# Kernel optimization log

Measured on AMD Instinct MI355X. Metric: run time of the kernel, lower is better.

The kernel has to match this reference:

```python
import jax, jax.numpy as jnp
import numpy as np

D_MODEL = 1024
NUM_HEADS = 16
HEAD_DIM = D_MODEL // NUM_HEADS


def setup_inputs() -> dict:
    key = jax.random.key(0)
    ks = jax.random.split(key, 11)
    B, S, D = 2, 2048, D_MODEL
    scale = 1.0 / np.sqrt(D)
    inp = {
        "query": jax.random.normal(ks[0], (B, S, D), jnp.float32),
        "key": jax.random.normal(ks[1], (B, S, D), jnp.float32),
        "value": jax.random.normal(ks[2], (B, S, D), jnp.float32),
        "Wq": jax.random.normal(ks[3], (D, D), jnp.float32) * scale,
        "bq": jnp.zeros((D,), jnp.float32),
        "Wk": jax.random.normal(ks[4], (D, D), jnp.float32) * scale,
        "bk": jnp.zeros((D,), jnp.float32),
        "Wv": jax.random.normal(ks[5], (D, D), jnp.float32) * scale,
        "bv": jnp.zeros((D,), jnp.float32),
        "Wo": jax.random.normal(ks[6], (D, D), jnp.float32) * scale,
        "bo": jnp.zeros((D,), jnp.float32),
    }
    return inp


def reference(query, key, value, Wq, bq, Wk, bk, Wv, bv, Wo, bo):
    B, S, D = query.shape
    H, hd = NUM_HEADS, HEAD_DIM
    # linear projections (x @ W^T + b, torch nn.Linear convention)
    Q = query @ Wq.T + bq
    K = key @ Wk.T + bk
    V = value @ Wv.T + bv
    # split heads: [B, S, H, hd] -> [B, H, S, hd]
    Q = Q.reshape(B, S, H, hd).transpose(0, 2, 1, 3)
    K = K.reshape(B, S, H, hd).transpose(0, 2, 1, 3)
    V = V.reshape(B, S, H, hd).transpose(0, 2, 1, 3)
    # scaled dot-product attention (explicit, non-flash)
    scores = jnp.einsum("bhqd,bhkd->bhqk", Q, K) / jnp.sqrt(jnp.float32(hd)).astype(Q.dtype)
    attn = jax.nn.softmax(scores, axis=-1)
    out = jnp.einsum("bhqk,bhkd->bhqd", attn, V)
    # merge heads: [B, H, S, hd] -> [B, S, D]
    out = out.transpose(0, 2, 1, 3).reshape(B, S, D)
    return out @ Wo.T + bo
```

## Files before the change

### kernel.cpp

```cpp
#include <hip/hip_runtime.h>
#include <hip/hip_bf16.h>


constexpr int D_MODEL = 1024;
constexpr int S_LEN   = 2048;
constexpr int BATCH   = 2;
constexpr int NH      = 16;
constexpr int HD      = 64;
constexpr int ROWS    = BATCH * S_LEN;

typedef __attribute__((ext_vector_type(8))) short short8;
typedef __attribute__((ext_vector_type(4))) float float4a;

static __device__ __forceinline__ unsigned short f2bf(float f) {
  union { float f; unsigned u; } v{f};
  unsigned r = v.u + 0x7FFFu + ((v.u >> 16) & 1u);
  return (unsigned short)(r >> 16);
}

static __device__ __forceinline__ unsigned pack_bf16(float a, float b) {
#if __has_builtin(__builtin_amdgcn_cvt_pk_bf16_f32)
  typedef __attribute__((ext_vector_type(2))) __bf16 bf16x2;
  union { bf16x2 v; unsigned u; } c;
  c.v = __builtin_amdgcn_cvt_pk_bf16_f32(a, b);
  return c.u;
#else
  return (unsigned)f2bf(a) | ((unsigned)f2bf(b) << 16);
#endif
}

static __device__ __forceinline__ float bf2f(unsigned short u) {
  union { unsigned u; float f; } v;
  v.u = (unsigned)u << 16;
  return v.f;
}

static __device__ __forceinline__ void async16(const void* g, void* l) {
  __builtin_amdgcn_global_load_lds(
      (const __attribute__((address_space(1))) unsigned int*)g,
      (__attribute__((address_space(3))) unsigned int*)l, 16, 0, 0);
}

struct ConvArgs { const float* s[7]; unsigned short* d[7]; int n[7]; };

__global__ __launch_bounds__(256) void convert_bf16(ConvArgs a) {
  const int which = blockIdx.y;
  const int i = (blockIdx.x * 256 + threadIdx.x) * 8;
  if (i >= a.n[which]) return;
  const float4* s = (const float4*)(a.s[which] + i);
  float4 x = s[0], y = s[1];
  unsigned t[4] = {pack_bf16(x.x, x.y), pack_bf16(x.z, x.w),
                   pack_bf16(y.x, y.y), pack_bf16(y.z, y.w)};
  *(short8*)(a.d[which] + i) = *(short8*)t;
}

template <int MODE>
static __device__ __forceinline__ void gemm_body(
    const unsigned short* __restrict__ A, const unsigned short* __restrict__ W,
    const float* __restrict__ bias, void* __restrict__ Yv, float scale,
    unsigned short* As, unsigned short* Bs, unsigned short* Tb) {
  const int tid = threadIdx.x;
  const int w = tid >> 6, lane = tid & 63;
  const int l15 = lane & 15, quad = lane >> 4;
  const int row0 = blockIdx.x * 128, col0 = blockIdx.y * 128;
  const int wm = (w & 1) * 64, wn = (w >> 1) * 64;

  float4a acc[4][4];
#pragma unroll
  for (int i = 0; i < 4; i++)
#pragma unroll
    for (int j = 0; j < 4; j++) acc[i][j] = (float4a){0.f, 0.f, 0.f, 0.f};

  const int swA = (quad + (wm >> 1) + (l15 >> 1)) & 3;
  const int swB = (quad + (wn >> 1) + (l15 >> 1)) & 3;

  for (int kt = 0; kt < D_MODEL; kt += 32) {
    __syncthreads();
#pragma unroll
    for (int j = 0; j < 2; j++) {
      const int i = w * 2 + j;
      const int r = i * 16 + (lane >> 2);
      const int c = ((lane & 3) - (r >> 1)) & 3;
      async16(W + (size_t)(col0 + r) * D_MODEL + kt + c * 8, (char*)Bs + i * 1024);
      async16(A + (size_t)(row0 + r) * D_MODEL + kt + c * 8, (char*)As + i * 1024);
    }
    __syncthreads();

    short8 af[4], bf[4];
#pragma unroll
    for (int mt = 0; mt < 4; mt++) {
      const int r = wm + mt * 16 + l15;
      af[mt] = *(const short8*)&As[(r * 4 + swA) * 8];
    }
#pragma unroll
    for (int nt = 0; nt < 4; nt++) {
      const int r = wn + nt * 16 + l15;
      bf[nt] = *(const short8*)&Bs[(r * 4 + swB) * 8];
    }
#pragma unroll
    for (int mt = 0; mt < 4; mt++)
#pragma unroll
      for (int nt = 0; nt < 4; nt++)
        acc[mt][nt] = __builtin_amdgcn_mfma_f32_16x16x32_bf16(af[mt], bf[nt], acc[mt][nt], 0, 0, 0);
  }

  int cols[4];
  float bvs[4];
#pragma unroll
  for (int nt = 0; nt < 4; nt++) {
    cols[nt] = col0 + wn + nt * 16 + l15;
    bvs[nt]  = bias[cols[nt]] * ((MODE == 0) ? scale : 1.0f);
  }

  if constexpr (MODE == 0) {
    unsigned short* Y = (unsigned short*)Yv;
#pragma unroll
    for (int mt = 0; mt < 4; mt++)
#pragma unroll
      for (int r = 0; r < 4; r++) {
        const int m = row0 + wm + mt * 16 + quad * 4 + r;
        const int bb = m >> 11, s = m & 2047;
#pragma unroll
        for (int nt = 0; nt < 4; nt++) {
          const int h = cols[nt] >> 6, d = cols[nt] & 63;
          Y[(((size_t)(bb * NH + h)) * S_LEN + s) * HD + d] =
              f2bf(acc[mt][nt][r] * scale + bvs[nt]);
        }
      }
  } else {
    __syncthreads();
    unsigned short* T = Tb + w * (64 * 32);
    unsigned short* Y = (unsigned short*)Yv;
#pragma unroll
    for (int p = 0; p < 2; p++) {
      if (p) { asm volatile("s_waitcnt lgkmcnt(0)" ::: "memory"); }
#pragma unroll
      for (int mi = 0; mi < 2; mi++) {
        const int mt = 2 * p + mi;
#pragma unroll
        for (int r = 0; r < 4; r++) {
          const int sl = mi * 16 + quad * 4 + r;
          const int cch = sl >> 3;
#pragma unroll
          for (int nt = 0; nt < 4; nt++) {
            const int dl = nt * 16 + l15;
            const int slot = cch ^ (dl & 3);
            T[dl * 32 + slot * 8 + (sl & 7)] = f2bf(acc[mt][nt][r] + bvs[nt]);
          }
        }
      }
      asm volatile("s_waitcnt lgkmcnt(0)" ::: "memory");
#pragma unroll
      for (int j = 0; j < 4; j++) {
        const int cid = j * 64 + lane;
        const int dl = cid >> 2;
        const int c  = cid & 3;
        const int slot = c ^ (dl & 3);
        short8 v = *(const short8*)&T[dl * 32 + slot * 8];
        const int col = col0 + wn + dl;
        const int h = col >> 6, d = col & 63;
        const int m = row0 + wm + p * 32 + c * 8;
        const int bb = m >> 11, s = m & 2047;
        *(short8*)&Y[(((size_t)(bb * NH + h)) * HD + d) * S_LEN + s] = v;
      }
    }
  }
}

__global__ __launch_bounds__(256) void gemm_qkv(
    const unsigned short* xq, const unsigned short* xk, const unsigned short* xv,
    const unsigned short* wq, const unsigned short* wk, const unsigned short* wv,
    const float* bq, const float* bk, const float* bv,
    unsigned short* Q, unsigned short* K, unsigned short* Vt) {
  __shared__ unsigned short smem[2 * 128 * 32];
  unsigned short* As = smem;
  unsigned short* Bs = smem + 128 * 32;
  unsigned short* Tb = smem;
  const int z = blockIdx.z;
  if (z == 0)      gemm_body<0>(xq, wq, bq, Q,  0.125f * 1.44269504f, As, Bs, Tb);
  else if (z == 1) gemm_body<0>(xk, wk, bk, K,  1.0f, As, Bs, Tb);
  else             gemm_body<2>(xv, wv, bv, Vt, 1.0f, As, Bs, Tb);
}

__global__ __launch_bounds__(256) void gemm_o(
    const unsigned short* __restrict__ Op, const float* __restrict__ Lp,
    const unsigned short* __restrict__ wo, const float* __restrict__ bo,
    float* __restrict__ out) {
  __shared__ unsigned short As[64 * 32];
  __shared__ unsigned short Bs[128 * 32];
  const int tid = threadIdx.x;
  const int w = tid >> 6, lane = tid & 63;
  const int l15 = lane & 15, quad = lane >> 4;
  const int row0 = blockIdx.x * 64, col0 = blockIdx.y * 128;
  const int wn = w * 32;

  const int ar = w * 16 + (lane >> 2);
  const int cg = lane & 3;
  const int asl = (cg + (ar >> 1)) & 3;
  const int grow = row0 + ar;
  const unsigned short* P0 = Op + (size_t)grow * D_MODEL + cg * 8;
  const unsigned short* P1 = P0 + (size_t)ROWS * D_MODEL;
  const float* L0 = Lp + (size_t)grow * NH;
  const float* L1 = L0 + (size_t)ROWS * NH;

  float4a acc[4][2];
#pragma unroll
  for (int i = 0; i < 4; i++)
#pragma unroll
    for (int j = 0; j < 2; j++) acc[i][j] = (float4a){0.f, 0.f, 0.f, 0.f};

  const int swA = (quad + (l15 >> 1)) & 3;
  const int swB = (quad + (wn >> 1) + (l15 >> 1)) & 3;

  for (int kt = 0; kt < D_MODEL; kt += 32) {
    const int h = kt >> 6;
    const float rinv = 1.0f / (L0[h] + L1[h]);
    short8 a = *(const short8*)(P0 + kt);
    short8 b = *(const short8*)(P1 + kt);
    unsigned t[4];
#pragma unroll
    for (int i = 0; i < 4; i++) {
      const float v0 = (bf2f((unsigned short)a[2 * i]) + bf2f((unsigned short)b[2 * i])) * rinv;
      const float v1 = (bf2f((unsigned short)a[2 * i + 1]) + bf2f((unsigned short)b[2 * i + 1])) * rinv;
      t[i] = pack_bf16(v0, v1);
    }
    __syncthreads();
    *(short8*)&As[(ar * 4 + asl) * 8] = *(short8*)t;
#pragma unroll
    for (int j = 0; j < 2; j++) {
      const int i = w * 2 + j;
      const int r = i * 16 + (lane >> 2);
      const int c = ((lane & 3) - (r >> 1)) & 3;
      async16(wo + (size_t)(col0 + r) * D_MODEL + kt + c * 8, (char*)Bs + i * 1024);
    }
    __syncthreads();

    short8 af[4], bf[2];
#pragma unroll
    for (int mt = 0; mt < 4; mt++) {
      const int r = mt * 16 + l15;
      af[mt] = *(const short8*)&As[(r * 4 + swA) * 8];
    }
#pragma unroll
    for (int nt = 0; nt < 2; nt++) {
      const int r = wn + nt * 16 + l15;
      bf[nt] = *(const short8*)&Bs[(r * 4 + swB) * 8];
    }
#pragma unroll
    for (int mt = 0; mt < 4; mt++)
#pragma unroll
      for (int nt = 0; nt < 2; nt++)
        acc[mt][nt] = __builtin_amdgcn_mfma_f32_16x16x32_bf16(af[mt], bf[nt], acc[mt][nt], 0, 0, 0);
  }

#pragma unroll
  for (int nt = 0; nt < 2; nt++) {
    const int col = col0 + wn + nt * 16 + l15;
    const float bv = bo[col];
#pragma unroll
    for (int mt = 0; mt < 4; mt++)
#pragma unroll
      for (int r = 0; r < 4; r++) {
        const int m = row0 + mt * 16 + quad * 4 + r;
        out[(size_t)m * D_MODEL + col] = acc[mt][nt][r] + bv;
      }
  }
}

__global__ __launch_bounds__(256) void attn_kernel(
    const unsigned short* __restrict__ Qh, const unsigned short* __restrict__ Kh,
    const unsigned short* __restrict__ Vt, unsigned short* __restrict__ Op,
    float* __restrict__ Lp) {
  const int qb = blockIdx.x;
  const int h  = blockIdx.y;
  const int bb = blockIdx.z >> 1, sp = blockIdx.z & 1;
  const int tid = threadIdx.x;
  const int w = tid >> 6, lane = tid & 63;
  const int l15 = lane & 15, quad = lane >> 4;

  __shared__ unsigned short Ks[64 * 64];
  __shared__ unsigned short Vs[64 * 64];
  __shared__ unsigned short Ps[4][32][72];

  const size_t bh = (size_t)(bb * NH + h);
  const unsigned short* Qp = Qh + bh * S_LEN * HD;
  const unsigned short* Kp = Kh + bh * S_LEN * HD;
  const unsigned short* Vp = Vt + bh * (size_t)HD * S_LEN;

  short8 qf[2][2];
#pragma unroll
  for (int qnt = 0; qnt < 2; qnt++)
#pragma unroll
    for (int c = 0; c < 2; c++)
      qf[qnt][c] = *(const short8*)(Qp + (size_t)(qb * 128 + w * 32 + qnt * 16 + l15) * HD +
                                    c * 32 + quad * 8);

  unsigned short ob[8] = {0x3F80, 0x3F80, 0x3F80, 0x3F80, 0x3F80, 0x3F80, 0x3F80, 0x3F80};
  const short8 ones = *(short8*)ob;

  float4a Oacc[2][4];
#pragma unroll
  for (int a = 0; a < 2; a++)
#pragma unroll
    for (int b = 0; b < 4; b++) Oacc[a][b] = (float4a){0.f, 0.f, 0.f, 0.f};
  float4a Lacc[2] = {(float4a){0.f, 0.f, 0.f, 0.f}, (float4a){0.f, 0.f, 0.f, 0.f}};

  const int sw0 = (quad + l15) & 7;
  const int sw1 = (quad + 4 + l15) & 7;

  for (int kb = sp * 1024; kb < sp * 1024 + 1024; kb += 64) {
    __syncthreads();
#pragma unroll
    for (int j = 0; j < 2; j++) {
      const int i = w * 2 + j;
      const int r = i * 8 + (lane >> 3);
      const int c = ((lane & 7) - r) & 7;
      async16(Kp + (size_t)(kb + r) * HD + c * 8, (char*)Ks + i * 1024);
      async16(Vp + (size_t)r * S_LEN + kb + c * 8, (char*)Vs + i * 1024);
    }
    __syncthreads();

#pragma unroll
    for (int mt = 0; mt < 4; mt++) {
      const int rb = (mt * 16 + l15) * 8;
      short8 a0 = *(const short8*)&Ks[(rb + sw0) * 8];
      short8 a1 = *(const short8*)&Ks[(rb + sw1) * 8];
#pragma unroll
      for (int qnt = 0; qnt < 2; qnt++) {
        float4a s = (float4a){0.f, 0.f, 0.f, 0.f};
        s = __builtin_amdgcn_mfma_f32_16x16x32_bf16(a0, qf[qnt][0], s, 0, 0, 0);
        s = __builtin_amdgcn_mfma_f32_16x16x32_bf16(a1, qf[qnt][1], s, 0, 0, 0);
        uint2 pk;
        pk.x = pack_bf16(__builtin_amdgcn_exp2f(s[0]), __builtin_amdgcn_exp2f(s[1]));
        pk.y = pack_bf16(__builtin_amdgcn_exp2f(s[2]), __builtin_amdgcn_exp2f(s[3]));
        *(uint2*)&Ps[w][qnt * 16 + l15][mt * 16 + quad * 4] = pk;
      }
    }
    asm volatile("s_waitcnt lgkmcnt(0)" ::: "memory");

#pragma unroll
    for (int c = 0; c < 2; c++) {
      short8 pa0 = *(const short8*)&Ps[w][l15][c * 32 + quad * 8];
      short8 pa1 = *(const short8*)&Ps[w][16 + l15][c * 32 + quad * 8];
      Lacc[0] = __builtin_amdgcn_mfma_f32_16x16x32_bf16(pa0, ones, Lacc[0], 0, 0, 0);
      Lacc[1] = __builtin_amdgcn_mfma_f32_16x16x32_bf16(pa1, ones, Lacc[1], 0, 0, 0);
      const int vsw = (c * 4 + quad + l15) & 7;
#pragma unroll
      for (int nt = 0; nt < 4; nt++) {
        short8 vb = *(const short8*)&Vs[((nt * 16 + l15) * 8 + vsw) * 8];
        Oacc[0][nt] = __builtin_amdgcn_mfma_f32_16x16x32_bf16(pa0, vb, Oacc[0][nt], 0, 0, 0);
        Oacc[1][nt] = __builtin_amdgcn_mfma_f32_16x16x32_bf16(pa1, vb, Oacc[1][nt], 0, 0, 0);
      }
    }
  }

  if (l15 == 0) {
#pragma unroll
    for (int qnt = 0; qnt < 2; qnt++)
#pragma unroll
      for (int reg = 0; reg < 4; reg++) {
        const int q = qb * 128 + w * 32 + qnt * 16 + quad * 4 + reg;
        Lp[(size_t)sp * ROWS * NH + ((size_t)bb * S_LEN + q) * NH + h] = Lacc[qnt][reg];
      }
  }

  unsigned short* Ob = Op + (size_t)sp * ROWS * D_MODEL;
#pragma unroll
  for (int qnt = 0; qnt < 2; qnt++) {
#pragma unroll
    for (int reg = 0; reg < 4; reg++) {
      const int q = qb * 128 + w * 32 + qnt * 16 + quad * 4 + reg;
      unsigned short* orow = Ob + ((size_t)bb * S_LEN + q) * D_MODEL + h * HD;
#pragma unroll
      for (int nt = 0; nt < 4; nt++)
        orow[nt * 16 + l15] = f2bf(Oacc[qnt][nt][reg]);
    }
  }
}

extern "C" void kernel_launch(void* const* d_in, const int* in_sizes, int n_in,
                              void* d_out, int out_size, void* d_ws, size_t ws_size,
                              hipStream_t stream) {
  const float* query = (const float*)d_in[0];
  const float* key   = (const float*)d_in[1];
  const float* value = (const float*)d_in[2];
  const float* Wq = (const float*)d_in[3];
  const float* bq = (const float*)d_in[4];
  const float* Wk = (const float*)d_in[5];
  const float* bk = (const float*)d_in[6];
  const float* Wv = (const float*)d_in[7];
  const float* bv = (const float*)d_in[8];
  const float* Wo = (const float*)d_in[9];
  const float* bo = (const float*)d_in[10];
  float* out = (float*)d_out;

  char* ws = (char*)d_ws;
  const size_t MB = 1024 * 1024;
  unsigned short* xq16 = (unsigned short*)(ws + 0 * MB);
  unsigned short* xk16 = (unsigned short*)(ws + 8 * MB);
  unsigned short* xv16 = (unsigned short*)(ws + 16 * MB);
  unsigned short* wq16 = (unsigned short*)(ws + 24 * MB);
  unsigned short* wk16 = (unsigned short*)(ws + 26 * MB);
  unsigned short* wv16 = (unsigned short*)(ws + 28 * MB);
  unsigned short* qbuf  = (unsigned short*)(ws + 32 * MB);
  unsigned short* kbuf  = (unsigned short*)(ws + 40 * MB);
  unsigned short* vtbuf = (unsigned short*)(ws + 48 * MB);
  unsigned short* wo16  = (unsigned short*)(ws + 56 * MB);
  float* Lp = (float*)(ws + 58 * MB);
  unsigned short* Op = (unsigned short*)(ws + 0 * MB);

  ConvArgs ca;
  const int NX = ROWS * D_MODEL, NW = D_MODEL * D_MODEL;
  ca.s[0] = query; ca.d[0] = xq16; ca.n[0] = NX;
  ca.s[1] = key;   ca.d[1] = xk16; ca.n[1] = NX;
  ca.s[2] = value; ca.d[2] = xv16; ca.n[2] = NX;
  ca.s[3] = Wq;    ca.d[3] = wq16; ca.n[3] = NW;
  ca.s[4] = Wk;    ca.d[4] = wk16; ca.n[4] = NW;
  ca.s[5] = Wv;    ca.d[5] = wv16; ca.n[5] = NW;
  ca.s[6] = Wo;    ca.d[6] = wo16; ca.n[6] = NW;
  hipLaunchKernelGGL(convert_bf16, dim3(NX / 2048, 7), dim3(256), 0, stream, ca);

  dim3 gqkv(ROWS / 128, D_MODEL / 128, 3);
  hipLaunchKernelGGL(gemm_qkv, gqkv, dim3(256), 0, stream,
                     xq16, xk16, xv16, wq16, wk16, wv16, bq, bk, bv,
                     qbuf, kbuf, vtbuf);

  dim3 ga(S_LEN / 128, NH, BATCH * 2);
  hipLaunchKernelGGL(attn_kernel, ga, dim3(256), 0, stream, qbuf, kbuf, vtbuf, Op, Lp);

  dim3 go(ROWS / 64, D_MODEL / 128);
  hipLaunchKernelGGL(gemm_o, go, dim3(256), 0, stream, Op, Lp, wo16, bo, out);
}
```

Measured before the change: 232.3 us.

## Fuse fp32-to-bf16 activation conversion into QKV GEMM and swizzle attention P buffer

The separate conversion pass over the query, key and value activations is removed. The QKV GEMM now loads fp32 activations directly, converts them in registers and stores them to LDS, with a register prefetch of the next K-slice. The standalone conversion kernel now handles only the four weight matrices, which cuts a full fp32 read and bf16 write/read round trip of the activations. Separately, the attention kernel's padded P staging buffer becomes an XOR-swizzled unpadded layout to avoid LDS bank conflicts. The trade-off is that the GEMM now reads twice the activation bytes per tile and converts them redundantly across the column blocks.

```diff
diff --git a/kernel.cpp b/kernel.cpp
--- a/kernel.cpp
+++ b/kernel.cpp
@@ -41,12 +41,11 @@
       (__attribute__((address_space(3))) unsigned int*)l, 16, 0, 0);
 }
 
-struct ConvArgs { const float* s[7]; unsigned short* d[7]; int n[7]; };
+struct ConvArgs { const float* s[4]; unsigned short* d[4]; };
 
 __global__ __launch_bounds__(256) void convert_bf16(ConvArgs a) {
   const int which = blockIdx.y;
   const int i = (blockIdx.x * 256 + threadIdx.x) * 8;
-  if (i >= a.n[which]) return;
   const float4* s = (const float4*)(a.s[which] + i);
   float4 x = s[0], y = s[1];
   unsigned t[4] = {pack_bf16(x.x, x.y), pack_bf16(x.z, x.w),
@@ -55,8 +54,8 @@
 }
 
 template <int MODE>
-static __device__ __forceinline__ void gemm_body(
-    const unsigned short* __restrict__ A, const unsigned short* __restrict__ W,
+static __device__ __forceinline__ void gemm_body_f(
+    const float* __restrict__ A32, const unsigned short* __restrict__ W,
     const float* __restrict__ bias, void* __restrict__ Yv, float scale,
     unsigned short* As, unsigned short* Bs, unsigned short* Tb) {
   const int tid = threadIdx.x;
@@ -65,26 +64,55 @@
   const int row0 = blockIdx.x * 128, col0 = blockIdx.y * 128;
   const int wm = (w & 1) * 64, wn = (w >> 1) * 64;
 
+  int rr[2], slotw[2];
+  const float* xptr[2];
+#pragma unroll
+  for (int j = 0; j < 2; j++) {
+    rr[j] = (w * 2 + j) * 16 + (lane >> 2);
+    slotw[j] = ((lane & 3) + (rr[j] >> 1)) & 3;
+    xptr[j] = A32 + (size_t)(row0 + rr[j]) * D_MODEL + (lane & 3) * 8;
+  }
+
+  float4 px[2][2];
+#pragma unroll
+  for (int j = 0; j < 2; j++) {
+    px[j][0] = ((const float4*)xptr[j])[0];
+    px[j][1] = ((const float4*)xptr[j])[1];
+  }
+
   float4a acc[4][4];
 #pragma unroll
   for (int i = 0; i < 4; i++)
 #pragma unroll
     for (int j = 0; j < 4; j++) acc[i][j] = (float4a){0.f, 0.f, 0.f, 0.f};
 
-  const int swA = (quad + (wm >> 1) + (l15 >> 1)) & 3;
-  const int swB = (quad + (wn >> 1) + (l15 >> 1)) & 3;
+  const int swA = (quad + (l15 >> 1)) & 3;
+  const int swB = (quad + (l15 >> 1)) & 3;
 
   for (int kt = 0; kt < D_MODEL; kt += 32) {
     __syncthreads();
+#pragma unroll
+    for (int j = 0; j < 2; j++) {
+      unsigned t[4] = {pack_bf16(px[j][0].x, px[j][0].y), pack_bf16(px[j][0].z, px[j][0].w),
+                       pack_bf16(px[j][1].x, px[j][1].y), pack_bf16(px[j][1].z, px[j][1].w)};
+      *(short8*)&As[(rr[j] * 4 + slotw[j]) * 8] = *(short8*)t;
+    }
 #pragma unroll
     for (int j = 0; j < 2; j++) {
       const int i = w * 2 + j;
       const int r = i * 16 + (lane >> 2);
       const int c = ((lane & 3) - (r >> 1)) & 3;
       async16(W + (size_t)(col0 + r) * D_MODEL + kt + c * 8, (char*)Bs + i * 1024);
-      async16(A + (size_t)(row0 + r) * D_MODEL + kt + c * 8, (char*)As + i * 1024);
-    }
-    __syncthreads();
+    }
+    __syncthreads();
+
+    if (kt + 32 < D_MODEL) {
+#pragma unroll
+      for (int j = 0; j < 2; j++) {
+        px[j][0] = ((const float4*)(xptr[j] + kt + 32))[0];
+        px[j][1] = ((const float4*)(xptr[j] + kt + 32))[1];
+      }
+    }
 
     short8 af[4], bf[4];
 #pragma unroll
@@ -168,7 +196,7 @@
 }
 
 __global__ __launch_bounds__(256) void gemm_qkv(
-    const unsigned short* xq, const unsigned short* xk, const unsigned short* xv,
+    const float* xq, const float* xk, const float* xv,
     const unsigned short* wq, const unsigned short* wk, const unsigned short* wv,
     const float* bq, const float* bk, const float* bv,
     unsigned short* Q, unsigned short* K, unsigned short* Vt) {
@@ -177,9 +205,9 @@
   unsigned short* Bs = smem + 128 * 32;
   unsigned short* Tb = smem;
   const int z = blockIdx.z;
-  if (z == 0)      gemm_body<0>(xq, wq, bq, Q,  0.125f * 1.44269504f, As, Bs, Tb);
-  else if (z == 1) gemm_body<0>(xk, wk, bk, K,  1.0f, As, Bs, Tb);
-  else             gemm_body<2>(xv, wv, bv, Vt, 1.0f, As, Bs, Tb);
+  if (z == 0)      gemm_body_f<0>(xq, wq, bq, Q,  0.125f * 1.44269504f, As, Bs, Tb);
+  else if (z == 1) gemm_body_f<0>(xk, wk, bk, K,  1.0f, As, Bs, Tb);
+  else             gemm_body_f<2>(xv, wv, bv, Vt, 1.0f, As, Bs, Tb);
 }
 
 __global__ __launch_bounds__(256) void gemm_o(
@@ -210,7 +238,7 @@
     for (int j = 0; j < 2; j++) acc[i][j] = (float4a){0.f, 0.f, 0.f, 0.f};
 
   const int swA = (quad + (l15 >> 1)) & 3;
-  const int swB = (quad + (wn >> 1) + (l15 >> 1)) & 3;
+  const int swB = (quad + (l15 >> 1)) & 3;
 
   for (int kt = 0; kt < D_MODEL; kt += 32) {
     const int h = kt >> 6;
@@ -280,7 +308,7 @@
 
   __shared__ unsigned short Ks[64 * 64];
   __shared__ unsigned short Vs[64 * 64];
-  __shared__ unsigned short Ps[4][32][72];
+  __shared__ unsigned short Ps[4][32 * 64];
 
   const size_t bh = (size_t)(bb * NH + h);
   const unsigned short* Qp = Qh + bh * S_LEN * HD;
@@ -307,6 +335,7 @@
 
   const int sw0 = (quad + l15) & 7;
   const int sw1 = (quad + 4 + l15) & 7;
+  const int l7 = l15 & 7;
 
   for (int kb = sp * 1024; kb < sp * 1024 + 1024; kb += 64) {
     __syncthreads();
@@ -325,6 +354,8 @@
       const int rb = (mt * 16 + l15) * 8;
       short8 a0 = *(const short8*)&Ks[(rb + sw0) * 8];
       short8 a1 = *(const short8*)&Ks[(rb + sw1) * 8];
+      const int chunk = mt * 2 + (quad >> 1);
+      const int woff = ((chunk ^ l7) * 8) + (quad & 1) * 4;
 #pragma unroll
       for (int qnt = 0; qnt < 2; qnt++) {
         float4a s = (float4a){0.f, 0.f, 0.f, 0.f};
@@ -333,15 +364,16 @@
         uint2 pk;
         pk.x = pack_bf16(__builtin_amdgcn_exp2f(s[0]), __builtin_amdgcn_exp2f(s[1]));
         pk.y = pack_bf16(__builtin_amdgcn_exp2f(s[2]), __builtin_amdgcn_exp2f(s[3]));
-        *(uint2*)&Ps[w][qnt * 16 + l15][mt * 16 + quad * 4] = pk;
+        *(uint2*)&Ps[w][(qnt * 16 + l15) * 64 + woff] = pk;
       }
     }
     asm volatile("s_waitcnt lgkmcnt(0)" ::: "memory");
 
 #pragma unroll
     for (int c = 0; c < 2; c++) {
-      short8 pa0 = *(const short8*)&Ps[w][l15][c * 32 + quad * 8];
-      short8 pa1 = *(const short8*)&Ps[w][16 + l15][c * 32 + quad * 8];
+      const int pslot = ((c * 4 + quad) ^ l7) * 8;
+      short8 pa0 = *(const short8*)&Ps[w][l15 * 64 + pslot];
+      short8 pa1 = *(const short8*)&Ps[w][(16 + l15) * 64 + pslot];
       Lacc[0] = __builtin_amdgcn_mfma_f32_16x16x32_bf16(pa0, ones, Lacc[0], 0, 0, 0);
       Lacc[1] = __builtin_amdgcn_mfma_f32_16x16x32_bf16(pa1, ones, Lacc[1], 0, 0, 0);
       const int vsw = (c * 4 + quad + l15) & 7;
@@ -396,33 +428,27 @@
 
   char* ws = (char*)d_ws;
   const size_t MB = 1024 * 1024;
-  unsigned short* xq16 = (unsigned short*)(ws + 0 * MB);
-  unsigned short* xk16 = (unsigned short*)(ws + 8 * MB);
-  unsigned short* xv16 = (unsigned short*)(ws + 16 * MB);
-  unsigned short* wq16 = (unsigned short*)(ws + 24 * MB);
-  unsigned short* wk16 = (unsigned short*)(ws + 26 * MB);
-  unsigned short* wv16 = (unsigned short*)(ws + 28 * MB);
-  unsigned short* qbuf  = (unsigned short*)(ws + 32 * MB);
-  unsigned short* kbuf  = (unsigned short*)(ws + 40 * MB);
-  unsigned short* vtbuf = (unsigned short*)(ws + 48 * MB);
-  unsigned short* wo16  = (unsigned short*)(ws + 56 * MB);
-  float* Lp = (float*)(ws + 58 * MB);
-  unsigned short* Op = (unsigned short*)(ws + 0 * MB);
+  unsigned short* wq16 = (unsigned short*)(ws + 0 * MB);
+  unsigned short* wk16 = (unsigned short*)(ws + 2 * MB);
+  unsigned short* wv16 = (unsigned short*)(ws + 4 * MB);
+  unsigned short* wo16 = (unsigned short*)(ws + 6 * MB);
+  unsigned short* qbuf  = (unsigned short*)(ws + 8 * MB);
+  unsigned short* kbuf  = (unsigned short*)(ws + 16 * MB);
+  unsigned short* vtbuf = (unsigned short*)(ws + 24 * MB);
+  unsigned short* Op    = (unsigned short*)(ws + 32 * MB);
+  float* Lp = (float*)(ws + 48 * MB);
 
   ConvArgs ca;
-  const int NX = ROWS * D_MODEL, NW = D_MODEL * D_MODEL;
-  ca.s[0] = query; ca.d[0] = xq16; ca.n[0] = NX;
-  ca.s[1] = key;   ca.d[1] = xk16; ca.n[1] = NX;
-  ca.s[2] = value; ca.d[2] = xv16; ca.n[2] = NX;
-  ca.s[3] = Wq;    ca.d[3] = wq16; ca.n[3] = NW;
-  ca.s[4] = Wk;    ca.d[4] = wk16; ca.n[4] = NW;
-  ca.s[5] = Wv;    ca.d[5] = wv16; ca.n[5] = NW;
-  ca.s[6] = Wo;    ca.d[6] = wo16; ca.n[6] = NW;
-  hipLaunchKernelGGL(convert_bf16, dim3(NX / 2048, 7), dim3(256), 0, stream, ca);
+  ca.s[0] = Wq; ca.d[0] = wq16;
+  ca.s[1] = Wk; ca.d[1] = wk16;
+  ca.s[2] = Wv; ca.d[2] = wv16;
+  ca.s[3] = Wo; ca.d[3] = wo16;
+  const int NW = D_MODEL * D_MODEL;
+  hipLaunchKernelGGL(convert_bf16, dim3(NW / 2048, 4), dim3(256), 0, stream, ca);
 
   dim3 gqkv(ROWS / 128, D_MODEL / 128, 3);
   hipLaunchKernelGGL(gemm_qkv, gqkv, dim3(256), 0, stream,
-                     xq16, xk16, xv16, wq16, wk16, wv16, bq, bk, bv,
+                     query, key, value, wq16, wk16, wv16, bq, bk, bv,
                      qbuf, kbuf, vtbuf);
 
   dim3 ga(S_LEN / 128, NH, BATCH * 2);
```

Result: slower. 287.4 us (+23.7%).
